# Kernel optimization log

Hardware: AMD Instinct MI355X
Metric: run time of the kernel (lower is better)

The kernel has to match this reference:

```python
import jax, jax.numpy as jnp
from jax import lax
import numpy as np
import math

B, H, W = 2, 48, 48
D_MODEL, D_STATE, D_CONV, EXPAND = 96, 16, 3, 2
D_INNER = EXPAND * D_MODEL
DT_RANK = math.ceil(D_MODEL / 16)
K = 6
L = H * W


def setup_inputs():
    key = jax.random.key(0)
    ks = jax.random.split(key, 10)
    x = jax.random.normal(ks[0], (B, H, W, D_MODEL), jnp.float32)
    y = jax.random.normal(ks[1], (B, H, W, D_MODEL), jnp.float32)
    k = jax.random.normal(ks[2], (B, H, W, D_MODEL), jnp.float32)
    in_proj_w = jax.random.normal(ks[3], (2 * D_INNER, D_MODEL), jnp.float32) * 0.02
    conv_w = jax.random.normal(ks[4], (D_INNER, 1, D_CONV, D_CONV), jnp.float32) * 0.1
    conv_b = jnp.zeros((D_INNER,), jnp.float32)
    x_proj_w = jax.random.normal(ks[5], (K, DT_RANK + 2 * D_STATE, D_INNER), jnp.float32) * 0.02
    s = DT_RANK ** -0.5
    dt_w = jax.random.uniform(ks[6], (K, D_INNER, DT_RANK), jnp.float32, -s, s)
    dt = jnp.exp(jax.random.uniform(ks[7], (K, D_INNER), jnp.float32)
                 * (math.log(0.1) - math.log(0.001)) + math.log(0.001))
    dt_b = dt + jnp.log(-jnp.expm1(-dt))  # inverse-softplus init as in dt_init
    A_logs = jnp.tile(jnp.log(jnp.arange(1, D_STATE + 1, dtype=jnp.float32))[None],
                      (K * D_INNER, 1))
    Ds = jnp.ones((K * D_INNER,), jnp.float32)
    ln_w = jnp.ones((D_INNER,), jnp.float32)
    ln_b = jnp.zeros((D_INNER,), jnp.float32)
    out_proj_w = jax.random.normal(ks[8], (D_MODEL, D_INNER), jnp.float32) * 0.02
    return dict(x=x, y=y, k=k, in_proj_w=in_proj_w, conv_w=conv_w, conv_b=conv_b,
                x_proj_w=x_proj_w, dt_w=dt_w, dt_b=dt_b, A_logs=A_logs, Ds=Ds,
                ln_w=ln_w, ln_b=ln_b, out_proj_w=out_proj_w)


def _diag_gather(t):
    # out[b,c,h,w] = t[b,c,h,(h+w)%W]; then (H,W)->(W,H) transpose, flatten
    idx = (jnp.arange(H)[:, None] + jnp.arange(W)[None, :]) % W
    g = jnp.take_along_axis(t, idx[None, None], axis=3)
    return jnp.swapaxes(g, -1, -2).reshape(t.shape[0], t.shape[1], L)


def _diag_scatter(flat):
    # inverse of _diag_gather: result[b,c,h,w] = r[b,c,h,(w-h)%W]
    r = jnp.swapaxes(flat.reshape(flat.shape[0], flat.shape[1], W, H), -1, -2)
    inv = (jnp.arange(W)[None, :] - jnp.arange(H)[:, None]) % W
    return jnp.take_along_axis(r, inv[None, None], axis=3)


def _forward(x, y, k, in_proj_w, conv_w, conv_b, x_proj_w, dt_w, dt_b,
             A_logs, Ds, ln_w, ln_b, out_proj_w):
    xv = jnp.einsum('bhwc,oc->bhwo', x, in_proj_w)[..., :D_INNER]
    yv = jnp.einsum('bhwc,oc->bhwo', y, in_proj_w)[..., :D_INNER]
    # NOTE: torch code overwrites z three times; the surviving gate z comes from k
    z = jnp.einsum('bhwc,oc->bhwo', k, in_proj_w)[..., D_INNER:]

    def conv_act(t):
        t = jnp.transpose(t, (0, 3, 1, 2))  # NCHW
        t = lax.conv_general_dilated(t, conv_w, (1, 1), ((1, 1), (1, 1)),
                                     feature_group_count=D_INNER,
                                     dimension_numbers=('NCHW', 'OIHW', 'NCHW'))
        return jax.nn.silu(t + conv_b[None, :, None, None])

    xc = conv_act(xv)  # (B,d,H,W)
    yc = conv_act(yv)

    h_x = xc.reshape(B, D_INNER, L)                                   # row-major
    v_y = jnp.swapaxes(yc, 2, 3).reshape(B, D_INNER, L)               # column-major
    diag_z = _diag_gather(yc)                                         # diagonal
    highfreq = jnp.stack([h_x, v_y, diag_z], axis=1)                  # (B,3,d,L)
    xs = jnp.concatenate([highfreq, jnp.flip(highfreq, axis=-1)], axis=1)  # (B,K,d,L)

    x_dbl = jnp.einsum('bkdl,kcd->bkcl', xs, x_proj_w)
    dts = jnp.einsum('bkrl,kdr->bkdl', x_dbl[:, :, :DT_RANK], dt_w)
    Bs = x_dbl[:, :, DT_RANK:DT_RANK + D_STATE]                       # (B,K,N,L)
    Cs = x_dbl[:, :, DT_RANK + D_STATE:]                              # (B,K,N,L)

    delta = jax.nn.softplus(dts + dt_b[None, :, :, None])             # (B,K,d,L)
    A = -jnp.exp(A_logs).reshape(K, D_INNER, D_STATE)
    Dk = Ds.reshape(K, D_INNER)

    def step(h, inp):
        dl, ul, Bl, Cl = inp  # (B,K,d),(B,K,d),(B,K,N),(B,K,N)
        h = jnp.exp(dl[..., None] * A) * h + (dl * ul)[..., None] * Bl[:, :, None, :]
        return h, jnp.einsum('bkdn,bkn->bkd', h, Cl)

    h0 = jnp.zeros((B, K, D_INNER, D_STATE), jnp.float32)
    seq = (jnp.moveaxis(delta, -1, 0), jnp.moveaxis(xs, -1, 0),
           jnp.moveaxis(Bs, -1, 0), jnp.moveaxis(Cs, -1, 0))
    _, ys = lax.scan(step, h0, seq)
    out_y = jnp.moveaxis(ys, 0, -1) + Dk[None, :, :, None] * xs       # (B,K,d,L)

    inv_y = jnp.flip(out_y[:, 3:6], axis=-1)

    def unT(t):  # undo the (W,H) raster used by vertical direction
        return jnp.swapaxes(t.reshape(B, D_INNER, W, H), -1, -2).reshape(B, D_INNER, L)

    y_h = out_y[:, 0] + inv_y[:, 0]
    y_v = unT(out_y[:, 1]) + unT(inv_y[:, 1])
    y_D = (_diag_scatter(out_y[:, 2]) + _diag_scatter(inv_y[:, 2])).reshape(B, D_INNER, L)

    zg = jax.nn.silu(z)

    def head(t):
        t = jnp.swapaxes(t, 1, 2).reshape(B, H, W, D_INNER)
        mu = t.mean(-1, keepdims=True)
        var = ((t - mu) ** 2).mean(-1, keepdims=True)
        t = (t - mu) * lax.rsqrt(var + 1e-5) * ln_w + ln_b
        return jnp.einsum('bhwd,od->bhwo', t * zg, out_proj_w)

    return head(y_h), head(y_v), head(y_D)


def reference(x, y, k, in_proj_w, conv_w, conv_b, x_proj_w, dt_w, dt_b,
              A_logs, Ds, ln_w, ln_b, out_proj_w):
    return _forward(x, y, k, in_proj_w, conv_w, conv_b, x_proj_w, dt_w, dt_b,
                    A_logs, Ds, ln_w, ln_b, out_proj_w)
```

## Files before the change

### kernel.cpp

```cpp
#include <hip/hip_runtime.h>
#include <hip/hip_bf16.h>

namespace {

constexpr int B_ = 2, H_ = 48, W_ = 48, DM_ = 96, DI_ = 192, NS_ = 16, RK_ = 6, K_ = 6;
constexpr int L_ = H_ * W_;
constexpr int C_ = 144;
constexpr int LC_ = L_ / C_;
constexpr int NPROJ = RK_ + 2 * NS_;
constexpr int NPAD = 48;

__device__ __forceinline__ float sigmoidf_(float x) { return 1.f / (1.f + __expf(-x)); }

__device__ __forceinline__ float delta_of(const float* __restrict__ dp,
                                          const float* __restrict__ wdt,
                                          float bias) {
  float s = bias;
#pragma unroll
  for (int r = 0; r < RK_; ++r) s += dp[r] * wdt[r];
  return (s > 20.f) ? s : __logf(1.f + __expf(s));
}

__global__ void k_prep(const float* __restrict__ Wp, const float* __restrict__ xpw,
                       const float* __restrict__ opw, const float* __restrict__ cw,
                       float* __restrict__ wInT, float* __restrict__ xpwT,
                       float* __restrict__ wT, float* __restrict__ cwT) {
  int blk = blockIdx.x;
  int tid = threadIdx.x;
  if (blk < DM_) {
    wInT[(size_t)blk * (2 * DI_) + tid] = Wp[(size_t)tid * DM_ + blk];
  } else if (blk < DM_ + K_) {
    int k = blk - DM_;
    if (tid < DI_) {
      float* dst = xpwT + ((size_t)k * DI_ + tid) * NPAD;
      for (int c = 0; c < NPAD; ++c)
        dst[c] = (c < NPROJ) ? xpw[((size_t)k * NPROJ + c) * DI_ + tid] : 0.f;
    }
  } else if (blk < DM_ + K_ + DI_) {
    int c = blk - DM_ - K_;
    if (tid < DM_)
      wT[(size_t)c * DM_ + tid] = opw[(size_t)tid * DI_ + c];
  } else {
    if (tid < DI_) {
#pragma unroll
      for (int j = 0; j < 9; ++j) cwT[j * DI_ + tid] = cw[tid * 9 + j];
    }
  }
}

constexpr int IM = 32, IBK = 32;
__global__ void __launch_bounds__(256) k_inproj2(
    const float* __restrict__ x, const float* __restrict__ y,
    const float* __restrict__ kin, const float* __restrict__ wInT,
    float* __restrict__ xv, float* __restrict__ yv, float* __restrict__ zg) {
  __shared__ float As[IM][IBK + 1];
  __shared__ float Ws[IBK][DI_ + 1];
  int tid = threadIdx.x;
  constexpr int BPS = (B_ * L_) / IM;
  int s = blockIdx.x / BPS;
  int row0 = (blockIdx.x % BPS) * IM;
  const float* src = (s == 0) ? x : (s == 1) ? y : kin;
  float* dst = (s == 0) ? xv : (s == 1) ? yv : zg;
  int nbase = (s == 2) ? DI_ : 0;
  int tm = tid >> 4, tn = tid & 15;
  float acc[2][12];
#pragma unroll
  for (int i = 0; i < 2; ++i)
#pragma unroll
    for (int j = 0; j < 12; ++j) acc[i][j] = 0.f;

  for (int k0 = 0; k0 < DM_; k0 += IBK) {
    {
      int r = tid >> 3, c4 = (tid & 7) << 2;
      const float4 v = *reinterpret_cast<const float4*>(
          &src[(size_t)(row0 + r) * DM_ + k0 + c4]);
      As[r][c4] = v.x; As[r][c4 + 1] = v.y; As[r][c4 + 2] = v.z; As[r][c4 + 3] = v.w;
    }
#pragma unroll
    for (int it = 0; it < 6; ++it) {
      int i = tid + it * 256;
      int r = i / 48, c4 = (i % 48) << 2;
      const float4 v = *reinterpret_cast<const float4*>(
          &wInT[(size_t)(k0 + r) * (2 * DI_) + nbase + c4]);
      Ws[r][c4] = v.x; Ws[r][c4 + 1] = v.y; Ws[r][c4 + 2] = v.z; Ws[r][c4 + 3] = v.w;
    }
    __syncthreads();
#pragma unroll
    for (int kk = 0; kk < IBK; ++kk) {
      float a0 = As[tm * 2 + 0][kk], a1 = As[tm * 2 + 1][kk];
      float w[12];
#pragma unroll
      for (int j = 0; j < 12; ++j) w[j] = Ws[kk][tn * 12 + j];
#pragma unroll
      for (int j = 0; j < 12; ++j) {
        acc[0][j] += a0 * w[j];
        acc[1][j] += a1 * w[j];
      }
    }
    __syncthreads();
  }
#pragma unroll
  for (int i = 0; i < 2; ++i) {
    size_t ob = (size_t)(row0 + tm * 2 + i) * DI_ + tn * 12;
#pragma unroll
    for (int j4 = 0; j4 < 3; ++j4) {
      float4 v;
      v.x = acc[i][j4 * 4 + 0]; v.y = acc[i][j4 * 4 + 1];
      v.z = acc[i][j4 * 4 + 2]; v.w = acc[i][j4 * 4 + 3];
      if (s == 2) {
        v.x *= sigmoidf_(v.x); v.y *= sigmoidf_(v.y);
        v.z *= sigmoidf_(v.z); v.w *= sigmoidf_(v.w);
      }
      *reinterpret_cast<float4*>(&dst[ob + j4 * 4]) = v;
    }
  }
}

__global__ void __launch_bounds__(192) k_conv_xs(
    const float* __restrict__ xv, const float* __restrict__ yv,
    const float* __restrict__ cwT, const float* __restrict__ cb,
    float* __restrict__ xs) {
  int tid = threadIdx.x;
  int p = tid / 48, q = tid % 48;
  int gl = blockIdx.x * 4 + p;
  int b = gl / L_, l = gl % L_;
  int h = l / W_, w = l % W_;
  int d4 = q << 2;
  float4 ax = *reinterpret_cast<const float4*>(&cb[d4]);
  float4 ay = ax;
#pragma unroll
  for (int kh = 0; kh < 3; ++kh) {
    int hh = h + kh - 1;
    if ((unsigned)hh >= (unsigned)H_) continue;
#pragma unroll
    for (int kw = 0; kw < 3; ++kw) {
      int ww = w + kw - 1;
      if ((unsigned)ww >= (unsigned)W_) continue;
      float4 wk = *reinterpret_cast<const float4*>(&cwT[(kh * 3 + kw) * DI_ + d4]);
      size_t idx = ((size_t)b * L_ + hh * W_ + ww) * DI_ + d4;
      float4 vx = *reinterpret_cast<const float4*>(&xv[idx]);
      float4 vy = *reinterpret_cast<const float4*>(&yv[idx]);
      ax.x += vx.x * wk.x; ax.y += vx.y * wk.y; ax.z += vx.z * wk.z; ax.w += vx.w * wk.w;
      ay.x += vy.x * wk.x; ay.y += vy.y * wk.y; ay.z += vy.z * wk.z; ay.w += vy.w * wk.w;
    }
  }
  ax.x *= sigmoidf_(ax.x); ax.y *= sigmoidf_(ax.y);
  ax.z *= sigmoidf_(ax.z); ax.w *= sigmoidf_(ax.w);
  ay.x *= sigmoidf_(ay.x); ay.y *= sigmoidf_(ay.y);
  ay.z *= sigmoidf_(ay.z); ay.w *= sigmoidf_(ay.w);
  size_t base = (size_t)b * K_ * L_;
  int lv = w * H_ + h;
  int lv2 = ((w - h + W_) % W_) * H_ + h;
#define STORE6(kk, pos, val) \
  *reinterpret_cast<float4*>(&xs[(base + (size_t)(kk) * L_ + (pos)) * DI_ + d4]) = (val)
  STORE6(0, l, ax);
  STORE6(3, L_ - 1 - l, ax);
  STORE6(1, lv, ay);
  STORE6(4, L_ - 1 - lv, ay);
  STORE6(2, lv2, ay);
  STORE6(5, L_ - 1 - lv2, ay);
#undef STORE6
}

constexpr int XM = 32, XBK = 32;
__global__ void __launch_bounds__(256) k_xdbl3(
    const float* __restrict__ xs, const float* __restrict__ xpwT,
    float* __restrict__ dts, float* __restrict__ Bsb, float* __restrict__ Csb) {
  __shared__ float As[XM][XBK + 1];
  __shared__ float Ws[XBK][NPAD];
  int tid = threadIdx.x;
  int row0 = blockIdx.x * XM;
  int k = (row0 / L_) % K_;
  int tm = tid >> 4, tn = tid & 15;
  float acc[2][3];
#pragma unroll
  for (int i = 0; i < 2; ++i)
#pragma unroll
    for (int j = 0; j < 3; ++j) acc[i][j] = 0.f;

  for (int k0 = 0; k0 < DI_; k0 += XBK) {
    {
      int r = tid >> 3, c4 = (tid & 7) << 2;
      const float4 v = *reinterpret_cast<const float4*>(
          &xs[(size_t)(row0 + r) * DI_ + k0 + c4]);
      As[r][c4] = v.x; As[r][c4 + 1] = v.y; As[r][c4 + 2] = v.z; As[r][c4 + 3] = v.w;
    }
#pragma unroll
    for (int it = 0; it < 2; ++it) {
      int i = tid + it * 256;
      if (i < 384) {
        int r = i / 12, c4 = (i % 12) << 2;
        const float4 v = *reinterpret_cast<const float4*>(
            &xpwT[((size_t)k * DI_ + k0 + r) * NPAD + c4]);
        Ws[r][c4] = v.x; Ws[r][c4 + 1] = v.y; Ws[r][c4 + 2] = v.z; Ws[r][c4 + 3] = v.w;
      }
    }
    __syncthreads();
#pragma unroll
    for (int kk = 0; kk < XBK; ++kk) {
      float a0 = As[tm * 2 + 0][kk], a1 = As[tm * 2 + 1][kk];
      float w0 = Ws[kk][tn * 3 + 0], w1 = Ws[kk][tn * 3 + 1], w2 = Ws[kk][tn * 3 + 2];
      acc[0][0] += a0 * w0; acc[0][1] += a0 * w1; acc[0][2] += a0 * w2;
      acc[1][0] += a1 * w0; acc[1][1] += a1 * w1; acc[1][2] += a1 * w2;
    }
    __syncthreads();
  }
#pragma unroll
  for (int i = 0; i < 2; ++i) {
    int row = row0 + tm * 2 + i;
#pragma unroll
    for (int j = 0; j < 3; ++j) {
      int cc = tn * 3 + j;
      float v = acc[i][j];
      if (cc < RK_) dts[(size_t)row * RK_ + cc] = v;
      else if (cc < RK_ + NS_) Bsb[(size_t)row * NS_ + (cc - RK_)] = v;
      else if (cc < NPROJ) Csb[(size_t)row * NS_ + (cc - RK_ - NS_)] = v;
    }
  }
}

__global__ void __launch_bounds__(192) k_scan1(
    const float* __restrict__ dts, const float* __restrict__ dtw,
    const float* __restrict__ dtb, const float* __restrict__ xs,
    const float* __restrict__ Bsb, const float* __restrict__ A_logs,
    float* __restrict__ Sdl, float* __restrict__ SHin) {
  int blk = blockIdx.x;
  int bk = blk / C_, c = blk % C_;
  int k = bk % K_;
  int d = threadIdx.x;
  float A[NS_];
#pragma unroll
  for (int n = 0; n < NS_; ++n) A[n] = -__expf(A_logs[((size_t)k * DI_ + d) * NS_ + n]);
  float wdt[RK_];
#pragma unroll
  for (int r = 0; r < RK_; ++r) wdt[r] = dtw[((size_t)k * DI_ + d) * RK_ + r];
  float bias = dtb[k * DI_ + d];
  float S[NS_];
#pragma unroll
  for (int n = 0; n < NS_; ++n) S[n] = 0.f;
  float sum_dl = 0.f;
  size_t base = (size_t)bk * L_ + (size_t)c * LC_;
  for (int l = 0; l < LC_; ++l) {
    float dl = delta_of(dts + (base + l) * RK_, wdt, bias);
    float u = xs[(base + l) * DI_ + d];
    float du = dl * u;
    sum_dl += dl;
    const float* Bp = Bsb + (base + l) * NS_;
#pragma unroll
    for (int n = 0; n < NS_; ++n) {
      float e = __expf(dl * A[n]);
      S[n] = e * S[n] + du * Bp[n];
    }
  }
  Sdl[(size_t)blk * DI_ + d] = sum_dl;
  size_t ob = (size_t)blk * NS_ * DI_ + d;
#pragma unroll
  for (int n = 0; n < NS_; ++n) SHin[ob + (size_t)n * DI_] = S[n];
}

__global__ void __launch_bounds__(192) k_scan2(
    const float* __restrict__ Sdl, const float* __restrict__ A_logs,
    float* __restrict__ SHin) {
  int bkn = blockIdx.x;
  int bk = bkn / NS_, n = bkn % NS_;
  int k = bk % K_;
  int d = threadIdx.x;
  float A = -__expf(A_logs[((size_t)k * DI_ + d) * NS_ + n]);
  float h = 0.f;
  for (int c = 0; c < C_; ++c) {
    size_t i = ((size_t)(bk * C_ + c) * NS_ + n) * DI_ + d;
    float s = SHin[i];
    float p = __expf(A * Sdl[(size_t)(bk * C_ + c) * DI_ + d]);
    SHin[i] = h;
    h = p * h + s;
  }
}

__global__ void __launch_bounds__(192) k_scan3(
    const float* __restrict__ dts, const float* __restrict__ dtw,
    const float* __restrict__ dtb, const float* __restrict__ xs,
    const float* __restrict__ Bsb, const float* __restrict__ Csb,
    const float* __restrict__ A_logs, const float* __restrict__ Ds,
    const float* __restrict__ SHin, float* __restrict__ out_y) {
  int blk = blockIdx.x;
  int bk = blk / C_, c = blk % C_;
  int k = bk % K_;
  int d = threadIdx.x;
  float A[NS_];
#pragma unroll
  for (int n = 0; n < NS_; ++n) A[n] = -__expf(A_logs[((size_t)k * DI_ + d) * NS_ + n]);
  float wdt[RK_];
#pragma unroll
  for (int r = 0; r < RK_; ++r) wdt[r] = dtw[((size_t)k * DI_ + d) * RK_ + r];
  float bias = dtb[k * DI_ + d];
  float Dk = Ds[k * DI_ + d];
  float h[NS_];
  size_t hb = (size_t)blk * NS_ * DI_ + d;
#pragma unroll
  for (int n = 0; n < NS_; ++n) h[n] = SHin[hb + (size_t)n * DI_];
  size_t base = (size_t)bk * L_ + (size_t)c * LC_;
  for (int l = 0; l < LC_; ++l) {
    float dl = delta_of(dts + (base + l) * RK_, wdt, bias);
    float u = xs[(base + l) * DI_ + d];
    float du = dl * u;
    const float* Bp = Bsb + (base + l) * NS_;
    const float* Cp = Csb + (base + l) * NS_;
    float yacc = 0.f;
#pragma unroll
    for (int n = 0; n < NS_; ++n) {
      h[n] = __expf(dl * A[n]) * h[n] + du * Bp[n];
      yacc += h[n] * Cp[n];
    }
    out_y[(base + l) * DI_ + d] = yacc + Dk * u;
  }
}

constexpr int MT = 32, GS_ = 196;
__global__ void __launch_bounds__(256) k_head2(
    const float* __restrict__ out_y, const float* __restrict__ zg,
    const float* __restrict__ lnw, const float* __restrict__ lnb,
    const float* __restrict__ wT, float* __restrict__ out) {
  __shared__ float Gs[MT][GS_];
  __shared__ float Ws[32][DM_ + 1];
  int tid = threadIdx.x;
  constexpr int BPS = (B_ * L_) / MT;
  int m = blockIdx.x / BPS;
  int r0 = (blockIdx.x % BPS) * MT;

  {
    int row = tid >> 3, t8 = tid & 7;
    int bl = r0 + row;
    int b = bl / L_, lp = bl % L_;
    int h = lp / W_, w = lp % W_;
    int l0;
    if (m == 0) l0 = lp;
    else if (m == 1) l0 = w * H_ + h;
    else l0 = ((w - h + W_) % W_) * H_ + h;
    size_t basef = ((size_t)b * K_ + m) * L_;
    size_t baser = ((size_t)b * K_ + m + 3) * L_;
    const float* pf = out_y + (basef + l0) * DI_;
    const float* pr = out_y + (baser + (size_t)(L_ - 1 - l0)) * DI_;
    float s = 0.f, s2 = 0.f;
#pragma unroll
    for (int j = 0; j < 6; ++j) {
      int c4 = t8 * 24 + j * 4;
      float4 a = *reinterpret_cast<const float4*>(&pf[c4]);
      float4 bb = *reinterpret_cast<const float4*>(&pr[c4]);
      float4 t;
      t.x = a.x + bb.x; t.y = a.y + bb.y; t.z = a.z + bb.z; t.w = a.w + bb.w;
      s += t.x + t.y + t.z + t.w;
      s2 += t.x * t.x + t.y * t.y + t.z * t.z + t.w * t.w;
      *reinterpret_cast<float4*>(&Gs[row][c4]) = t;
    }
    s += __shfl_xor(s, 1, 64);  s2 += __shfl_xor(s2, 1, 64);
    s += __shfl_xor(s, 2, 64);  s2 += __shfl_xor(s2, 2, 64);
    s += __shfl_xor(s, 4, 64);  s2 += __shfl_xor(s2, 4, 64);
    float mu = s * (1.f / DI_);
    float var = fmaxf(s2 * (1.f / DI_) - mu * mu, 0.f);
    float rs = rsqrtf(var + 1e-5f);
    const float* zp = zg + (size_t)bl * DI_;
#pragma unroll
    for (int j = 0; j < 6; ++j) {
      int c4 = t8 * 24 + j * 4;
      float4 t = *reinterpret_cast<const float4*>(&Gs[row][c4]);
      float4 zv = *reinterpret_cast<const float4*>(&zp[c4]);
      t.x = ((t.x - mu) * rs * lnw[c4 + 0] + lnb[c4 + 0]) * zv.x;
      t.y = ((t.y - mu) * rs * lnw[c4 + 1] + lnb[c4 + 1]) * zv.y;
      t.z = ((t.z - mu) * rs * lnw[c4 + 2] + lnb[c4 + 2]) * zv.z;
      t.w = ((t.w - mu) * rs * lnw[c4 + 3] + lnb[c4 + 3]) * zv.w;
      *reinterpret_cast<float4*>(&Gs[row][c4]) = t;
    }
  }
  __syncthreads();

  int tm = tid >> 4, tn = tid & 15;
  float acc[2][6];
#pragma unroll
  for (int i = 0; i < 2; ++i)
#pragma unroll
    for (int j = 0; j < 6; ++j) acc[i][j] = 0.f;

  for (int k0 = 0; k0 < DI_; k0 += 32) {
#pragma unroll
    for (int it = 0; it < 3; ++it) {
      int i = tid + it * 256;
      int r = i / 24, c4 = (i % 24) << 2;
      const float4 v = *reinterpret_cast<const float4*>(
          &wT[(size_t)(k0 + r) * DM_ + c4]);
      Ws[r][c4] = v.x; Ws[r][c4 + 1] = v.y; Ws[r][c4 + 2] = v.z; Ws[r][c4 + 3] = v.w;
    }
    __syncthreads();
#pragma unroll
    for (int kk = 0; kk < 32; ++kk) {
      float a0 = Gs[tm * 2 + 0][k0 + kk], a1 = Gs[tm * 2 + 1][k0 + kk];
      float w[6];
#pragma unroll
      for (int j = 0; j < 6; ++j) w[j] = Ws[kk][tn * 6 + j];
#pragma unroll
      for (int j = 0; j < 6; ++j) {
        acc[0][j] += a0 * w[j];
        acc[1][j] += a1 * w[j];
      }
    }
    __syncthreads();
  }
  size_t obase = ((size_t)m * (B_ * L_) + r0) * DM_;
#pragma unroll
  for (int i = 0; i < 2; ++i) {
    size_t ob = obase + (size_t)(tm * 2 + i) * DM_ + tn * 6;
#pragma unroll
    for (int j = 0; j < 6; ++j) out[ob + j] = acc[i][j];
  }
}

}

extern "C" void kernel_launch(void* const* d_in, const int* in_sizes, int n_in,
                              void* d_out, int out_size, void* d_ws, size_t ws_size,
                              hipStream_t stream) {
  const float* x = (const float*)d_in[0];
  const float* y = (const float*)d_in[1];
  const float* kin = (const float*)d_in[2];
  const float* in_proj_w = (const float*)d_in[3];
  const float* conv_w = (const float*)d_in[4];
  const float* conv_b = (const float*)d_in[5];
  const float* x_proj_w = (const float*)d_in[6];
  const float* dt_w = (const float*)d_in[7];
  const float* dt_b = (const float*)d_in[8];
  const float* A_logs = (const float*)d_in[9];
  const float* Ds = (const float*)d_in[10];
  const float* ln_w = (const float*)d_in[11];
  const float* ln_b = (const float*)d_in[12];
  const float* out_proj_w = (const float*)d_in[13];
  float* out = (float*)d_out;

  float* ws = (float*)d_ws;
  const size_t BLD = (size_t)B_ * L_ * DI_;
  const size_t BKLD = (size_t)B_ * K_ * L_ * DI_;
  const size_t BKLN = (size_t)B_ * K_ * L_ * NS_;
  const size_t PSN = (size_t)B_ * K_ * C_ * NS_ * DI_;
  float* xv = ws;             ws += BLD;
  float* yv = ws;             ws += BLD;
  float* zg = ws;             ws += BLD;
  float* xs = ws;             ws += BKLD;
  float* Bsb = ws;            ws += BKLN;
  float* Csb = ws;            ws += BKLN;
  float* out_y = ws;          ws += BKLD;
  float* SHin = ws;           ws += PSN;
  float* Sdl = ws;            ws += (size_t)B_ * K_ * C_ * DI_;
  float* wT = ws;             ws += (size_t)DI_ * DM_;
  float* xpwT = ws;           ws += (size_t)K_ * DI_ * NPAD;
  float* wInT = ws;           ws += (size_t)DM_ * 2 * DI_;
  float* dts = ws;            ws += (size_t)B_ * K_ * L_ * RK_;
  float* cwT = ws;            ws += (size_t)9 * DI_;

  k_prep<<<DM_ + K_ + DI_ + 1, 384, 0, stream>>>(in_proj_w, x_proj_w, out_proj_w,
                                                 conv_w, wInT, xpwT, wT, cwT);
  k_inproj2<<<3 * B_ * L_ / IM, 256, 0, stream>>>(x, y, kin, wInT, xv, yv, zg);
  k_conv_xs<<<B_ * L_ / 4, 192, 0, stream>>>(xv, yv, cwT, conv_b, xs);
  k_xdbl3<<<B_ * K_ * L_ / XM, 256, 0, stream>>>(xs, xpwT, dts, Bsb, Csb);
  k_scan1<<<B_ * K_ * C_, 192, 0, stream>>>(dts, dt_w, dt_b, xs, Bsb, A_logs, Sdl, SHin);
  k_scan2<<<B_ * K_ * NS_, 192, 0, stream>>>(Sdl, A_logs, SHin);
  k_scan3<<<B_ * K_ * C_, 192, 0, stream>>>(dts, dt_w, dt_b, xs, Bsb, Csb, A_logs,
                                            Ds, SHin, out_y);
  k_head2<<<3 * B_ * L_ / MT, 256, 0, stream>>>(out_y, zg, ln_w, ln_b, wT, out);
}
```

Measured before the change: 172.6 us.

## Drop weight-transpose prep kernel and stage scan B/C/dt chunks in shared memory

Removes the k_prep launch. The GEMM kernels now read the original row-major weights and transpose them while storing into shared-memory tiles, and the conv kernel transposes its 3x3 weights into LDS in every block. The scan kernels also preload each chunk's B, C and dt rows into shared memory instead of reading them through global pointers on every step. This saves one launch and the global round trip for the transposed weights. In exchange, the shared-memory stores are strided, which may cause bank conflicts, and every conv block repeats the weight transpose.

```diff
diff --git a/kernel.cpp b/kernel.cpp
--- a/kernel.cpp
+++ b/kernel.cpp
@@ -21,37 +21,10 @@
   return (s > 20.f) ? s : __logf(1.f + __expf(s));
 }
 
-__global__ void k_prep(const float* __restrict__ Wp, const float* __restrict__ xpw,
-                       const float* __restrict__ opw, const float* __restrict__ cw,
-                       float* __restrict__ wInT, float* __restrict__ xpwT,
-                       float* __restrict__ wT, float* __restrict__ cwT) {
-  int blk = blockIdx.x;
-  int tid = threadIdx.x;
-  if (blk < DM_) {
-    wInT[(size_t)blk * (2 * DI_) + tid] = Wp[(size_t)tid * DM_ + blk];
-  } else if (blk < DM_ + K_) {
-    int k = blk - DM_;
-    if (tid < DI_) {
-      float* dst = xpwT + ((size_t)k * DI_ + tid) * NPAD;
-      for (int c = 0; c < NPAD; ++c)
-        dst[c] = (c < NPROJ) ? xpw[((size_t)k * NPROJ + c) * DI_ + tid] : 0.f;
-    }
-  } else if (blk < DM_ + K_ + DI_) {
-    int c = blk - DM_ - K_;
-    if (tid < DM_)
-      wT[(size_t)c * DM_ + tid] = opw[(size_t)tid * DI_ + c];
-  } else {
-    if (tid < DI_) {
-#pragma unroll
-      for (int j = 0; j < 9; ++j) cwT[j * DI_ + tid] = cw[tid * 9 + j];
-    }
-  }
-}
-
 constexpr int IM = 32, IBK = 32;
 __global__ void __launch_bounds__(256) k_inproj2(
     const float* __restrict__ x, const float* __restrict__ y,
-    const float* __restrict__ kin, const float* __restrict__ wInT,
+    const float* __restrict__ kin, const float* __restrict__ inpw,
     float* __restrict__ xv, float* __restrict__ yv, float* __restrict__ zg) {
   __shared__ float As[IM][IBK + 1];
   __shared__ float Ws[IBK][DI_ + 1];
@@ -79,10 +52,11 @@
 #pragma unroll
     for (int it = 0; it < 6; ++it) {
       int i = tid + it * 256;
-      int r = i / 48, c4 = (i % 48) << 2;
+      int col = i >> 3, k4 = (i & 7) << 2;
       const float4 v = *reinterpret_cast<const float4*>(
-          &wInT[(size_t)(k0 + r) * (2 * DI_) + nbase + c4]);
-      Ws[r][c4] = v.x; Ws[r][c4 + 1] = v.y; Ws[r][c4 + 2] = v.z; Ws[r][c4 + 3] = v.w;
+          &inpw[(size_t)(nbase + col) * DM_ + k0 + k4]);
+      Ws[k4 + 0][col] = v.x; Ws[k4 + 1][col] = v.y;
+      Ws[k4 + 2][col] = v.z; Ws[k4 + 3][col] = v.w;
     }
     __syncthreads();
 #pragma unroll
@@ -118,9 +92,15 @@
 
 __global__ void __launch_bounds__(192) k_conv_xs(
     const float* __restrict__ xv, const float* __restrict__ yv,
-    const float* __restrict__ cwT, const float* __restrict__ cb,
+    const float* __restrict__ cw, const float* __restrict__ cb,
     float* __restrict__ xs) {
+  __shared__ float scw[9 * DI_];
   int tid = threadIdx.x;
+  for (int i = tid; i < 9 * DI_; i += 192) {
+    int d = i / 9, j = i % 9;
+    scw[j * DI_ + d] = cw[i];
+  }
+  __syncthreads();
   int p = tid / 48, q = tid % 48;
   int gl = blockIdx.x * 4 + p;
   int b = gl / L_, l = gl % L_;
@@ -136,7 +116,7 @@
     for (int kw = 0; kw < 3; ++kw) {
       int ww = w + kw - 1;
       if ((unsigned)ww >= (unsigned)W_) continue;
-      float4 wk = *reinterpret_cast<const float4*>(&cwT[(kh * 3 + kw) * DI_ + d4]);
+      float4 wk = *reinterpret_cast<const float4*>(&scw[(kh * 3 + kw) * DI_ + d4]);
       size_t idx = ((size_t)b * L_ + hh * W_ + ww) * DI_ + d4;
       float4 vx = *reinterpret_cast<const float4*>(&xv[idx]);
       float4 vy = *reinterpret_cast<const float4*>(&yv[idx]);
@@ -164,7 +144,7 @@
 
 constexpr int XM = 32, XBK = 32;
 __global__ void __launch_bounds__(256) k_xdbl3(
-    const float* __restrict__ xs, const float* __restrict__ xpwT,
+    const float* __restrict__ xs, const float* __restrict__ xpw,
     float* __restrict__ dts, float* __restrict__ Bsb, float* __restrict__ Csb) {
   __shared__ float As[XM][XBK + 1];
   __shared__ float Ws[XBK][NPAD];
@@ -172,6 +152,10 @@
   int row0 = blockIdx.x * XM;
   int k = (row0 / L_) % K_;
   int tm = tid >> 4, tn = tid & 15;
+  for (int i = tid; i < XBK * (NPAD - NPROJ); i += 256) {
+    int kk = i / (NPAD - NPROJ), c = NPROJ + i % (NPAD - NPROJ);
+    Ws[kk][c] = 0.f;
+  }
   float acc[2][3];
 #pragma unroll
   for (int i = 0; i < 2; ++i)
@@ -188,11 +172,12 @@
 #pragma unroll
     for (int it = 0; it < 2; ++it) {
       int i = tid + it * 256;
-      if (i < 384) {
-        int r = i / 12, c4 = (i % 12) << 2;
+      if (i < NPROJ * 8) {
+        int c = i >> 3, k4 = (i & 7) << 2;
         const float4 v = *reinterpret_cast<const float4*>(
-            &xpwT[((size_t)k * DI_ + k0 + r) * NPAD + c4]);
-        Ws[r][c4] = v.x; Ws[r][c4 + 1] = v.y; Ws[r][c4 + 2] = v.z; Ws[r][c4 + 3] = v.w;
+            &xpw[((size_t)k * NPROJ + c) * DI_ + k0 + k4]);
+        Ws[k4 + 0][c] = v.x; Ws[k4 + 1][c] = v.y;
+        Ws[k4 + 2][c] = v.z; Ws[k4 + 3][c] = v.w;
       }
     }
     __syncthreads();
@@ -224,10 +209,15 @@
     const float* __restrict__ dtb, const float* __restrict__ xs,
     const float* __restrict__ Bsb, const float* __restrict__ A_logs,
     float* __restrict__ Sdl, float* __restrict__ SHin) {
+  __shared__ float sB[LC_ * NS_];
+  __shared__ float sdt[LC_ * RK_];
   int blk = blockIdx.x;
   int bk = blk / C_, c = blk % C_;
   int k = bk % K_;
   int d = threadIdx.x;
+  size_t base = (size_t)bk * L_ + (size_t)c * LC_;
+  for (int i = d; i < LC_ * NS_; i += 192) sB[i] = Bsb[base * NS_ + i];
+  for (int i = d; i < LC_ * RK_; i += 192) sdt[i] = dts[base * RK_ + i];
   float A[NS_];
 #pragma unroll
   for (int n = 0; n < NS_; ++n) A[n] = -__expf(A_logs[((size_t)k * DI_ + d) * NS_ + n]);
@@ -239,13 +229,13 @@
 #pragma unroll
   for (int n = 0; n < NS_; ++n) S[n] = 0.f;
   float sum_dl = 0.f;
-  size_t base = (size_t)bk * L_ + (size_t)c * LC_;
+  __syncthreads();
   for (int l = 0; l < LC_; ++l) {
-    float dl = delta_of(dts + (base + l) * RK_, wdt, bias);
+    float dl = delta_of(&sdt[l * RK_], wdt, bias);
     float u = xs[(base + l) * DI_ + d];
     float du = dl * u;
     sum_dl += dl;
-    const float* Bp = Bsb + (base + l) * NS_;
+    const float* Bp = &sB[l * NS_];
 #pragma unroll
     for (int n = 0; n < NS_; ++n) {
       float e = __expf(dl * A[n]);
@@ -282,10 +272,19 @@
     const float* __restrict__ Bsb, const float* __restrict__ Csb,
     const float* __restrict__ A_logs, const float* __restrict__ Ds,
     const float* __restrict__ SHin, float* __restrict__ out_y) {
+  __shared__ float sB[LC_ * NS_];
+  __shared__ float sC[LC_ * NS_];
+  __shared__ float sdt[LC_ * RK_];
   int blk = blockIdx.x;
   int bk = blk / C_, c = blk % C_;
   int k = bk % K_;
   int d = threadIdx.x;
+  size_t base = (size_t)bk * L_ + (size_t)c * LC_;
+  for (int i = d; i < LC_ * NS_; i += 192) {
+    sB[i] = Bsb[base * NS_ + i];
+    sC[i] = Csb[base * NS_ + i];
+  }
+  for (int i = d; i < LC_ * RK_; i += 192) sdt[i] = dts[base * RK_ + i];
   float A[NS_];
 #pragma unroll
   for (int n = 0; n < NS_; ++n) A[n] = -__expf(A_logs[((size_t)k * DI_ + d) * NS_ + n]);
@@ -298,13 +297,13 @@
   size_t hb = (size_t)blk * NS_ * DI_ + d;
 #pragma unroll
   for (int n = 0; n < NS_; ++n) h[n] = SHin[hb + (size_t)n * DI_];
-  size_t base = (size_t)bk * L_ + (size_t)c * LC_;
+  __syncthreads();
   for (int l = 0; l < LC_; ++l) {
-    float dl = delta_of(dts + (base + l) * RK_, wdt, bias);
+    float dl = delta_of(&sdt[l * RK_], wdt, bias);
     float u = xs[(base + l) * DI_ + d];
     float du = dl * u;
-    const float* Bp = Bsb + (base + l) * NS_;
-    const float* Cp = Csb + (base + l) * NS_;
+    const float* Bp = &sB[l * NS_];
+    const float* Cp = &sC[l * NS_];
     float yacc = 0.f;
 #pragma unroll
     for (int n = 0; n < NS_; ++n) {
@@ -319,7 +318,7 @@
 __global__ void __launch_bounds__(256) k_head2(
     const float* __restrict__ out_y, const float* __restrict__ zg,
     const float* __restrict__ lnw, const float* __restrict__ lnb,
-    const float* __restrict__ wT, float* __restrict__ out) {
+    const float* __restrict__ opw, float* __restrict__ out) {
   __shared__ float Gs[MT][GS_];
   __shared__ float Ws[32][DM_ + 1];
   int tid = threadIdx.x;
@@ -384,10 +383,11 @@
 #pragma unroll
     for (int it = 0; it < 3; ++it) {
       int i = tid + it * 256;
-      int r = i / 24, c4 = (i % 24) << 2;
+      int o = i >> 3, k4 = (i & 7) << 2;
       const float4 v = *reinterpret_cast<const float4*>(
-          &wT[(size_t)(k0 + r) * DM_ + c4]);
-      Ws[r][c4] = v.x; Ws[r][c4 + 1] = v.y; Ws[r][c4 + 2] = v.z; Ws[r][c4 + 3] = v.w;
+          &opw[(size_t)o * DI_ + k0 + k4]);
+      Ws[k4 + 0][o] = v.x; Ws[k4 + 1][o] = v.y;
+      Ws[k4 + 2][o] = v.z; Ws[k4 + 3][o] = v.w;
     }
     __syncthreads();
 #pragma unroll
@@ -439,29 +439,23 @@
   const size_t BKLD = (size_t)B_ * K_ * L_ * DI_;
   const size_t BKLN = (size_t)B_ * K_ * L_ * NS_;
   const size_t PSN = (size_t)B_ * K_ * C_ * NS_ * DI_;
-  float* xv = ws;             ws += BLD;
-  float* yv = ws;             ws += BLD;
-  float* zg = ws;             ws += BLD;
-  float* xs = ws;             ws += BKLD;
-  float* Bsb = ws;            ws += BKLN;
-  float* Csb = ws;            ws += BKLN;
-  float* out_y = ws;          ws += BKLD;
-  float* SHin = ws;           ws += PSN;
-  float* Sdl = ws;            ws += (size_t)B_ * K_ * C_ * DI_;
-  float* wT = ws;             ws += (size_t)DI_ * DM_;
-  float* xpwT = ws;           ws += (size_t)K_ * DI_ * NPAD;
-  float* wInT = ws;           ws += (size_t)DM_ * 2 * DI_;
-  float* dts = ws;            ws += (size_t)B_ * K_ * L_ * RK_;
-  float* cwT = ws;            ws += (size_t)9 * DI_;
-
-  k_prep<<<DM_ + K_ + DI_ + 1, 384, 0, stream>>>(in_proj_w, x_proj_w, out_proj_w,
-                                                 conv_w, wInT, xpwT, wT, cwT);
-  k_inproj2<<<3 * B_ * L_ / IM, 256, 0, stream>>>(x, y, kin, wInT, xv, yv, zg);
-  k_conv_xs<<<B_ * L_ / 4, 192, 0, stream>>>(xv, yv, cwT, conv_b, xs);
-  k_xdbl3<<<B_ * K_ * L_ / XM, 256, 0, stream>>>(xs, xpwT, dts, Bsb, Csb);
+  float* xv = ws;     ws += BLD;
+  float* yv = ws;     ws += BLD;
+  float* zg = ws;     ws += BLD;
+  float* xs = ws;     ws += BKLD;
+  float* Bsb = ws;    ws += BKLN;
+  float* Csb = ws;    ws += BKLN;
+  float* out_y = ws;  ws += BKLD;
+  float* SHin = ws;   ws += PSN;
+  float* Sdl = ws;    ws += (size_t)B_ * K_ * C_ * DI_;
+  float* dts = ws;    ws += (size_t)B_ * K_ * L_ * RK_;
+
+  k_inproj2<<<3 * B_ * L_ / IM, 256, 0, stream>>>(x, y, kin, in_proj_w, xv, yv, zg);
+  k_conv_xs<<<B_ * L_ / 4, 192, 0, stream>>>(xv, yv, conv_w, conv_b, xs);
+  k_xdbl3<<<B_ * K_ * L_ / XM, 256, 0, stream>>>(xs, x_proj_w, dts, Bsb, Csb);
   k_scan1<<<B_ * K_ * C_, 192, 0, stream>>>(dts, dt_w, dt_b, xs, Bsb, A_logs, Sdl, SHin);
   k_scan2<<<B_ * K_ * NS_, 192, 0, stream>>>(Sdl, A_logs, SHin);
   k_scan3<<<B_ * K_ * C_, 192, 0, stream>>>(dts, dt_w, dt_b, xs, Bsb, Csb, A_logs,
                                             Ds, SHin, out_y);
-  k_head2<<<3 * B_ * L_ / MT, 256, 0, stream>>>(out_y, zg, ln_w, ln_b, wT, out);
-}
+  k_head2<<<3 * B_ * L_ / MT, 256, 0, stream>>>(out_y, zg, ln_w, ln_b, out_proj_w, out);
+}
```

After: 162.6 us. -5.8%, faster.
